# Kernel tuning notes

Measured on AMD Instinct MI355X. Metric: run time of the kernel, lower is better.

The kernel has to match this reference:

```python
import jax, jax.numpy as jnp
import numpy as np


def setup_inputs() -> dict:
    key = jax.random.key(0)
    k1, k2 = jax.random.split(key)
    B, S, D = 4, 2048, 128
    x = jax.random.normal(k1, (B, S, D), dtype=jnp.float32)
    concept_map = jax.random.normal(k2, (D, D, D), dtype=jnp.float32) * 0.02
    return {"x": x, "concept_map": concept_map}


def reference(x, concept_map):
    # x: [B, S, D]; concept_map: [D, D, D]
    B, S, D = x.shape
    DECAY = jnp.asarray(1.2, x.dtype)

    # Decayed running sum: s_i = (s_{i-1} + x_{i-1}) / 1.2, s_0 = 0.
    def step(c, xt):
        c = (c + xt) / DECAY
        return c, c

    _, s = jax.lax.scan(step, jnp.zeros((B, D), x.dtype), jnp.swapaxes(x[:, :-1], 0, 1))
    s = jnp.swapaxes(s, 0, 1)                                   # [B, S-1, D]
    s = jnp.concatenate([jnp.zeros((B, 1, D), x.dtype), s], 1)  # [B, S, D]; step 0 contributes zeros

    # conceptual_matrix[b,s] = outer(x[b,s], s[b,s]); result[b,s,f] = sum_{d,e} cm[b,s,d,e] * W[f,d,e]
    # (dropout is identity at inference)
    return jnp.einsum('bsd,bse,fde->bsf', x, s, concept_map, optimize=True)
```

## Files before the change

kernel.cpp:

```cpp
#include <hip/hip_runtime.h>

typedef _Float16 f16;
typedef _Float16 f16x2 __attribute__((ext_vector_type(2)));
typedef _Float16 f16x8 __attribute__((ext_vector_type(8)));
typedef float f32x4 __attribute__((ext_vector_type(4)));
typedef unsigned int u32;
typedef unsigned int u32x4 __attribute__((ext_vector_type(4)));

static __device__ __forceinline__ u32 pk2(float lo, float hi) {
  union { f16 h[2]; u32 u; } v;
  v.h[0] = (f16)lo; v.h[1] = (f16)hi;
  return v.u;
}

__global__ void k_pre(const float* __restrict__ W, char* __restrict__ wt,
                      const float* __restrict__ x, float* __restrict__ st) {
  int bid = blockIdx.x;
  if (bid < 2048) {
    int t = bid * 256 + threadIdx.x;
    long i = (long)t * 4;
    int f = (int)(i >> 14);
    int k = (int)(i & 16383);
    float4 w4 = *(const float4*)(W + i);
    int d = k >> 7, e = k & 127;
    long byo = (long)d * 32768 + (e >> 5) * 8192 + f * 64 + ((e >> 3) & 3) * 16 + (e & 7) * 2;
    u32* dst = (u32*)(wt + byo);
    dst[0] = pk2(w4.x, w4.y);
    dst[1] = pk2(w4.z, w4.w);
  } else {
    int tid = (bid - 2048) * 256 + threadIdx.x;
    int e  = tid & 127;
    int bc = tid >> 7;
    int b  = bc >> 5;
    int ch = bc & 31;
    int t0 = ch * 64;
    const float* xb = x + (long)b * 2048 * 128 + e;
    float* sb = st + (long)e * 8192 + b * 2048;
    const float inv = 1.0f / 1.2f;
    float c = 0.f;
    if (ch > 0) {
      const float* xp = xb + (long)(t0 - 64) * 128;
      #pragma unroll
      for (int t = 0; t < 64; ++t) c = (c + xp[t * 128]) * inv;
    }
    const float* xq = xb + (long)t0 * 128;
    float* sq = sb + t0;
    #pragma unroll
    for (int t = 0; t < 64; ++t) { sq[t] = c; c = (c + xq[t * 128]) * inv; }
  }
}

__global__ void k_red(const float4* __restrict__ part, float4* __restrict__ out) {
  int i = blockIdx.x * 256 + threadIdx.x;
  float4 a = part[i];
  float4 b = part[i + 262144];
  float4 c = part[i + 524288];
  float4 d = part[i + 786432];
  out[i] = make_float4(a.x + b.x + c.x + d.x, a.y + b.y + c.y + d.y,
                       a.z + b.z + c.z + d.z, a.w + b.w + c.w + d.w);
}

__global__ __launch_bounds__(512, 2) void k_main(
    const float* __restrict__ x, const float* __restrict__ st,
    const char* __restrict__ wt, float* __restrict__ part) {
  __shared__ u32 x_lds[128 * 36];
  __shared__ float red[128 * 129];

  const int tid  = threadIdx.x;
  const int bid  = blockIdx.x;
  const int kq   = bid & 3;
  const int tt   = bid >> 2;
  const int wv   = tid >> 6;
  const int lane = tid & 63;
  const int ng   = wv & 1;
  const int ep   = wv >> 1;
  const int r    = lane & 15;
  const int kg   = lane >> 4;
  const int tokenBase = tt * 128;

  {
    int row = tid >> 2, c0 = (tid & 3) * 8;
    const float* src = x + (long)(tokenBase + row) * 128 + kq * 32 + c0;
    float4 v0 = *(const float4*)src;
    float4 v1 = *(const float4*)(src + 4);
    u32* dst = &x_lds[row * 36 + c0];
    dst[0] = pk2(v0.x, v0.x); dst[1] = pk2(v0.y, v0.y);
    dst[2] = pk2(v0.z, v0.z); dst[3] = pk2(v0.w, v0.w);
    dst[4] = pk2(v1.x, v1.x); dst[5] = pk2(v1.y, v1.y);
    dst[6] = pk2(v1.z, v1.z); dst[7] = pk2(v1.w, v1.w);
  }

  u32 sreg[8][4];
  {
    const float* stb = st + tokenBase + (long)(ep * 32 + kg * 8) * 8192;
    #pragma unroll
    for (int mr = 0; mr < 8; ++mr)
      #pragma unroll
      for (int jj = 0; jj < 4; ++jj) {
        const float* qp = stb + (long)(2 * jj) * 8192 + mr * 16 + r;
        sreg[mr][jj] = pk2(qp[0], qp[8192]);
      }
  }
  __syncthreads();

  f32x4 acc[8][4];
  #pragma unroll
  for (int mr = 0; mr < 8; ++mr)
    #pragma unroll
    for (int n = 0; n < 4; ++n) acc[mr][n] = (f32x4){0.f, 0.f, 0.f, 0.f};

  const int loff = r * 64 + kg * 16;
  const char* wtq = wt + (long)(kq * 32) * 32768 + ep * 8192 + ng * 4096;

#define STEP(BUF, XB, J)                                                     \
  {                                                                          \
    _Pragma("unroll")                                                        \
    for (int mr = 0; mr < 8; ++mr) {                                         \
      f16x2 xv2;                                                             \
      *(u32*)&xv2 = XB[mr][J];                                               \
      union { u32 u[4]; f16x8 v; } au;                                       \
      _Pragma("unroll")                                                      \
      for (int jj = 0; jj < 4; ++jj) {                                       \
        f16x2 s2;                                                            \
        *(u32*)&s2 = sreg[mr][jj];                                           \
        f16x2 p = xv2 * s2;                                                  \
        au.u[jj] = *(u32*)&p;                                                \
      }                                                                      \
      _Pragma("unroll")                                                      \
      for (int n = 0; n < 4; ++n)                                            \
        acc[mr][n] = __builtin_amdgcn_mfma_f32_16x16x32_f16(                 \
            au.v, BUF[n], acc[mr][n], 0, 0, 0);                              \
    }                                                                        \
  }
#define BLOAD(BUF, IT)                                                       \
  {                                                                          \
    int itc = (IT) > 31 ? 31 : (IT);                                         \
    const char* wn = wtq + (long)itc * 32768;                                \
    _Pragma("unroll")                                                        \
    for (int n = 0; n < 4; ++n)                                              \
      BUF[n] = *(const f16x8*)(wn + n * 1024 + loff);                        \
  }

  f16x8 ba[4], bb[4];
  BLOAD(ba, 0);

  #pragma unroll 1
  for (int it4 = 0; it4 < 8; ++it4) {
    u32x4 xb[8];
    #pragma unroll
    for (int mr = 0; mr < 8; ++mr)
      xb[mr] = *(const u32x4*)&x_lds[(mr * 16 + r) * 36 + it4 * 4];
    int it = it4 * 4;
    BLOAD(bb, it + 1); STEP(ba, xb, 0);
    BLOAD(ba, it + 2); STEP(bb, xb, 1);
    BLOAD(bb, it + 3); STEP(ba, xb, 2);
    BLOAD(ba, it + 4); STEP(bb, xb, 3);
  }
#undef STEP
#undef BLOAD

  __syncthreads();
  #pragma unroll
  for (int round = 0; round < 4; ++round) {
    if (ep == round) {
      #pragma unroll
      for (int mr = 0; mr < 8; ++mr)
        #pragma unroll
        for (int n = 0; n < 4; ++n)
          #pragma unroll
          for (int q2 = 0; q2 < 4; ++q2) {
            int idx = (mr * 16 + kg * 4 + q2) * 129 + ng * 64 + n * 16 + r;
            if (round == 0) red[idx] = acc[mr][n][q2];
            else            red[idx] += acc[mr][n][q2];
          }
    }
    __syncthreads();
  }
  float* outp = part + (long)kq * 1048576 + (long)tokenBase * 128;
  #pragma unroll
  for (int j = 0; j < 32; ++j) {
    int row = (tid >> 7) + j * 4;
    int col = tid & 127;
    outp[row * 128 + col] = red[row * 129 + col];
  }
}

extern "C" void kernel_launch(void* const* d_in, const int* in_sizes, int n_in,
                              void* d_out, int out_size, void* d_ws, size_t ws_size,
                              hipStream_t stream) {
  const float* x = (const float*)d_in[0];
  const float* W = (const float*)d_in[1];
  float* out  = (float*)d_out;
  float* st   = (float*)d_ws;
  char*  wt   = (char*)d_ws + (4 << 20);
  float* part = (float*)((char*)d_ws + (8 << 20));

  k_pre <<<dim3(2112), dim3(256), 0, stream>>>(W, wt, x, st);
  k_main<<<dim3(256),  dim3(512), 0, stream>>>(x, st, wt, part);
  k_red <<<dim3(1024), dim3(256), 0, stream>>>((const float4*)part, (float4*)out);
}
```

Before: 53.82 us.

## Stream weight tiles through LDS with async global_load_lds triple buffering

Replaces the register double-buffered global loads of the fp16 weight fragments with per-wave asynchronous global-to-LDS copies (global_load_lds) into a three-slot ring. Each wave waits on vmcnt for its current slot, then reads the fragments from LDS. MFMA sections are wrapped in s_setprio. The aim is to keep two weight tiles in flight and hide global load latency behind the MFMA work without tying up VGPRs. In exchange, LDS usage grows (the reduction buffer now aliases the staging ring) and each tile costs an extra LDS round trip.

```diff
diff --git a/kernel.cpp b/kernel.cpp
--- a/kernel.cpp
+++ b/kernel.cpp
@@ -6,6 +6,9 @@
 typedef float f32x4 __attribute__((ext_vector_type(4)));
 typedef unsigned int u32;
 typedef unsigned int u32x4 __attribute__((ext_vector_type(4)));
+
+#define AS1 __attribute__((address_space(1)))
+#define AS3 __attribute__((address_space(3)))
 
 static __device__ __forceinline__ u32 pk2(float lo, float hi) {
   union { f16 h[2]; u32 u; } v;
@@ -63,8 +66,9 @@
 __global__ __launch_bounds__(512, 2) void k_main(
     const float* __restrict__ x, const float* __restrict__ st,
     const char* __restrict__ wt, float* __restrict__ part) {
-  __shared__ u32 x_lds[128 * 36];
-  __shared__ float red[128 * 129];
+  __shared__ __attribute__((aligned(128))) char lds[18432 + 8 * 3 * 4096];
+  u32* x_lds  = (u32*)lds;
+  float* red  = (float*)(lds + 18432);
 
   const int tid  = threadIdx.x;
   const int bid  = blockIdx.x;
@@ -109,15 +113,36 @@
     #pragma unroll
     for (int n = 0; n < 4; ++n) acc[mr][n] = (f32x4){0.f, 0.f, 0.f, 0.f};
 
-  const int loff = r * 64 + kg * 16;
   const char* wtq = wt + (long)(kq * 32) * 32768 + ep * 8192 + ng * 4096;
-
-#define STEP(BUF, XB, J)                                                     \
+  char* bslot = lds + 18432 + wv * 12288;
+  const int lsub = r * 64 + kg * 16;
+
+#define DMA(SLOT, IT)                                                        \
   {                                                                          \
+    const char* gs = wtq + (long)(IT) * 32768;                               \
+    char* ls = bslot + (SLOT) * 4096;                                        \
+    _Pragma("unroll")                                                        \
+    for (int q = 0; q < 4; ++q)                                              \
+      __builtin_amdgcn_global_load_lds(                                      \
+          (const AS1 u32*)(gs + q * 1024 + lane * 16),                       \
+          (AS3 u32*)(ls + q * 1024 + lane * 16), 16, 0, 0);                  \
+  }
+#define PHASE(IT, J)                                                         \
+  {                                                                          \
+    __builtin_amdgcn_sched_barrier(0);                                       \
+    int nt = (IT) + 2 > 31 ? 31 : (IT) + 2;                                  \
+    DMA(((IT) + 2) % 3, nt);                                                 \
+    __asm__ __volatile__("s_waitcnt vmcnt(8)" ::: "memory");                 \
+    const char* bs = bslot + ((IT) % 3) * 4096;                              \
+    f16x8 bfr[4];                                                            \
+    _Pragma("unroll")                                                        \
+    for (int n = 0; n < 4; ++n)                                              \
+      bfr[n] = *(const f16x8*)(bs + n * 1024 + lsub);                        \
+    __builtin_amdgcn_s_setprio(1);                                           \
     _Pragma("unroll")                                                        \
     for (int mr = 0; mr < 8; ++mr) {                                         \
       f16x2 xv2;                                                             \
-      *(u32*)&xv2 = XB[mr][J];                                               \
+      *(u32*)&xv2 = xb[mr][J];                                               \
       union { u32 u[4]; f16x8 v; } au;                                       \
       _Pragma("unroll")                                                      \
       for (int jj = 0; jj < 4; ++jj) {                                       \
@@ -129,20 +154,13 @@
       _Pragma("unroll")                                                      \
       for (int n = 0; n < 4; ++n)                                            \
         acc[mr][n] = __builtin_amdgcn_mfma_f32_16x16x32_f16(                 \
-            au.v, BUF[n], acc[mr][n], 0, 0, 0);                              \
+            au.v, bfr[n], acc[mr][n], 0, 0, 0);                              \
     }                                                                        \
-  }
-#define BLOAD(BUF, IT)                                                       \
-  {                                                                          \
-    int itc = (IT) > 31 ? 31 : (IT);                                         \
-    const char* wn = wtq + (long)itc * 32768;                                \
-    _Pragma("unroll")                                                        \
-    for (int n = 0; n < 4; ++n)                                              \
-      BUF[n] = *(const f16x8*)(wn + n * 1024 + loff);                        \
-  }
-
-  f16x8 ba[4], bb[4];
-  BLOAD(ba, 0);
+    __builtin_amdgcn_s_setprio(0);                                           \
+  }
+
+  DMA(0, 0);
+  DMA(1, 1);
 
   #pragma unroll 1
   for (int it4 = 0; it4 < 8; ++it4) {
@@ -151,13 +169,13 @@
     for (int mr = 0; mr < 8; ++mr)
       xb[mr] = *(const u32x4*)&x_lds[(mr * 16 + r) * 36 + it4 * 4];
     int it = it4 * 4;
-    BLOAD(bb, it + 1); STEP(ba, xb, 0);
-    BLOAD(ba, it + 2); STEP(bb, xb, 1);
-    BLOAD(bb, it + 3); STEP(ba, xb, 2);
-    BLOAD(ba, it + 4); STEP(bb, xb, 3);
-  }
-#undef STEP
-#undef BLOAD
+    PHASE(it, 0);
+    PHASE(it + 1, 1);
+    PHASE(it + 2, 2);
+    PHASE(it + 3, 3);
+  }
+#undef PHASE
+#undef DMA
 
   __syncthreads();
   #pragma unroll
```

After: 54.68 us. Within noise of the previous version (+1.6%).

## Switch main GEMM from 16x16x32 to 32x32x16 MFMA tiles

Applied to the files above, without the earlier changes.

Replaces the 16x16x32 f16 MFMA tiling with 32x32x16 MFMA, remapping the per-lane state registers, the x LDS reads, the weight fragment loads and the accumulator-to-LDS reduction indices to the 32x32 layout. Larger MFMA tiles halve the number of A-operand products and MFMA issues per k-step and reduce the x/s elementwise multiply work per MFMA. The cost is a different accumulator layout, which risks reduction bank conflicts, plus possible differences in MFMA throughput.

```diff
diff --git a/kernel.cpp b/kernel.cpp
--- a/kernel.cpp
+++ b/kernel.cpp
@@ -3,7 +3,7 @@
 typedef _Float16 f16;
 typedef _Float16 f16x2 __attribute__((ext_vector_type(2)));
 typedef _Float16 f16x8 __attribute__((ext_vector_type(8)));
-typedef float f32x4 __attribute__((ext_vector_type(4)));
+typedef float f32x16 __attribute__((ext_vector_type(16)));
 typedef unsigned int u32;
 typedef unsigned int u32x4 __attribute__((ext_vector_type(4)));
 
@@ -74,8 +74,8 @@
   const int lane = tid & 63;
   const int ng   = wv & 1;
   const int ep   = wv >> 1;
-  const int r    = lane & 15;
-  const int kg   = lane >> 4;
+  const int l31  = lane & 31;
+  const int hi   = lane >> 5;
   const int tokenBase = tt * 128;
 
   {
@@ -90,66 +90,74 @@
     dst[6] = pk2(v1.z, v1.z); dst[7] = pk2(v1.w, v1.w);
   }
 
-  u32 sreg[8][4];
+  u32 sreg[4][2][4];
   {
-    const float* stb = st + tokenBase + (long)(ep * 32 + kg * 8) * 8192;
-    #pragma unroll
-    for (int mr = 0; mr < 8; ++mr)
-      #pragma unroll
-      for (int jj = 0; jj < 4; ++jj) {
-        const float* qp = stb + (long)(2 * jj) * 8192 + mr * 16 + r;
-        sreg[mr][jj] = pk2(qp[0], qp[8192]);
-      }
+    #pragma unroll
+    for (int m = 0; m < 4; ++m)
+      #pragma unroll
+      for (int kk = 0; kk < 2; ++kk)
+        #pragma unroll
+        for (int jj = 0; jj < 4; ++jj) {
+          const float* qp = st + (long)(ep * 32 + kk * 16 + hi * 8 + 2 * jj) * 8192
+                              + tokenBase + m * 32 + l31;
+          sreg[m][kk][jj] = pk2(qp[0], qp[8192]);
+        }
   }
   __syncthreads();
 
-  f32x4 acc[8][4];
+  f32x16 acc[4][2];
   #pragma unroll
-  for (int mr = 0; mr < 8; ++mr)
-    #pragma unroll
-    for (int n = 0; n < 4; ++n) acc[mr][n] = (f32x4){0.f, 0.f, 0.f, 0.f};
-
-  const int loff = r * 64 + kg * 16;
+  for (int m = 0; m < 4; ++m)
+    #pragma unroll
+    for (int n = 0; n < 2; ++n)
+      #pragma unroll
+      for (int q = 0; q < 16; ++q) acc[m][n][q] = 0.f;
+
   const char* wtq = wt + (long)(kq * 32) * 32768 + ep * 8192 + ng * 4096;
-
-#define STEP(BUF, XB, J)                                                     \
-  {                                                                          \
-    _Pragma("unroll")                                                        \
-    for (int mr = 0; mr < 8; ++mr) {                                         \
-      f16x2 xv2;                                                             \
-      *(u32*)&xv2 = XB[mr][J];                                               \
-      union { u32 u[4]; f16x8 v; } au;                                       \
-      _Pragma("unroll")                                                      \
-      for (int jj = 0; jj < 4; ++jj) {                                       \
-        f16x2 s2;                                                            \
-        *(u32*)&s2 = sreg[mr][jj];                                           \
-        f16x2 p = xv2 * s2;                                                  \
-        au.u[jj] = *(u32*)&p;                                                \
-      }                                                                      \
-      _Pragma("unroll")                                                      \
-      for (int n = 0; n < 4; ++n)                                            \
-        acc[mr][n] = __builtin_amdgcn_mfma_f32_16x16x32_f16(                 \
-            au.v, BUF[n], acc[mr][n], 0, 0, 0);                              \
-    }                                                                        \
-  }
+  const int lboff = l31 * 64 + hi * 16;
+
 #define BLOAD(BUF, IT)                                                       \
   {                                                                          \
     int itc = (IT) > 31 ? 31 : (IT);                                         \
     const char* wn = wtq + (long)itc * 32768;                                \
+    BUF[0][0] = *(const f16x8*)(wn + lboff);                                 \
+    BUF[0][1] = *(const f16x8*)(wn + 2048 + lboff);                          \
+    BUF[1][0] = *(const f16x8*)(wn + 32 + lboff);                            \
+    BUF[1][1] = *(const f16x8*)(wn + 2048 + 32 + lboff);                     \
+  }
+#define STEP(BUF, XB, J)                                                     \
+  {                                                                          \
     _Pragma("unroll")                                                        \
-    for (int n = 0; n < 4; ++n)                                              \
-      BUF[n] = *(const f16x8*)(wn + n * 1024 + loff);                        \
-  }
-
-  f16x8 ba[4], bb[4];
+    for (int kk = 0; kk < 2; ++kk) {                                         \
+      _Pragma("unroll")                                                      \
+      for (int m = 0; m < 4; ++m) {                                          \
+        f16x2 xv2;                                                           \
+        *(u32*)&xv2 = XB[m][J];                                              \
+        union { u32 u[4]; f16x8 v; } au;                                     \
+        _Pragma("unroll")                                                    \
+        for (int jj = 0; jj < 4; ++jj) {                                     \
+          f16x2 s2;                                                          \
+          *(u32*)&s2 = sreg[m][kk][jj];                                      \
+          f16x2 p = xv2 * s2;                                                \
+          au.u[jj] = *(u32*)&p;                                              \
+        }                                                                    \
+        acc[m][0] = __builtin_amdgcn_mfma_f32_32x32x16_f16(                  \
+            au.v, BUF[kk][0], acc[m][0], 0, 0, 0);                           \
+        acc[m][1] = __builtin_amdgcn_mfma_f32_32x32x16_f16(                  \
+            au.v, BUF[kk][1], acc[m][1], 0, 0, 0);                           \
+      }                                                                      \
+    }                                                                        \
+  }
+
+  f16x8 ba[2][2], bb[2][2];
   BLOAD(ba, 0);
 
   #pragma unroll 1
   for (int it4 = 0; it4 < 8; ++it4) {
-    u32x4 xb[8];
-    #pragma unroll
-    for (int mr = 0; mr < 8; ++mr)
-      xb[mr] = *(const u32x4*)&x_lds[(mr * 16 + r) * 36 + it4 * 4];
+    u32x4 xb[4];
+    #pragma unroll
+    for (int m = 0; m < 4; ++m)
+      xb[m] = *(const u32x4*)&x_lds[(m * 32 + l31) * 36 + it4 * 4];
     int it = it4 * 4;
     BLOAD(bb, it + 1); STEP(ba, xb, 0);
     BLOAD(ba, it + 2); STEP(bb, xb, 1);
@@ -164,14 +172,15 @@
   for (int round = 0; round < 4; ++round) {
     if (ep == round) {
       #pragma unroll
-      for (int mr = 0; mr < 8; ++mr)
+      for (int m = 0; m < 4; ++m)
         #pragma unroll
-        for (int n = 0; n < 4; ++n)
+        for (int n = 0; n < 2; ++n)
           #pragma unroll
-          for (int q2 = 0; q2 < 4; ++q2) {
-            int idx = (mr * 16 + kg * 4 + q2) * 129 + ng * 64 + n * 16 + r;
-            if (round == 0) red[idx] = acc[mr][n][q2];
-            else            red[idx] += acc[mr][n][q2];
+          for (int reg = 0; reg < 16; ++reg) {
+            int token = m * 32 + (reg & 3) + 8 * (reg >> 2) + 4 * hi;
+            int idx = token * 129 + ng * 64 + n * 32 + l31;
+            if (round == 0) red[idx] = acc[m][n][reg];
+            else            red[idx] += acc[m][n][reg];
           }
     }
     __syncthreads();
```

Measured after the change: 57.29 us. 6.4% more time.
